# Optimization experiments

Measured on AMD Instinct MI355X. Metric: run time of the kernel, lower is better.

## Reference

```python
import jax, jax.numpy as jnp
import numpy as np

B, L, I, H, O = 32, 4096, 128, 256, 128
DELAY = 4  # delay-line length is DELAY+1


def setup_inputs() -> dict:
    key = jax.random.key(0)
    ks = jax.random.split(key, 9)
    s = 0.02
    return {
        "x": jax.random.normal(ks[0], (B, L, I), jnp.float32),
        # MGRUCell params (minimal-GRU: forget gate uses delayed state)
        "Wz": jax.random.normal(ks[1], (I, H), jnp.float32) * s,
        "Uz": jax.random.normal(ks[2], (H, H), jnp.float32) * s,
        "bz": jnp.zeros((H,), jnp.float32),
        "Wh": jax.random.normal(ks[3], (I, H), jnp.float32) * s,
        "Uh": jax.random.normal(ks[4], (H, H), jnp.float32) * s,
        "bh": jnp.zeros((H,), jnp.float32),
        # head: Linear(H, O)
        "Wo": jax.random.normal(ks[5], (H, O), jnp.float32) * s,
        "bo": jnp.zeros((O,), jnp.float32),
    }


def reference(x, Wz, Uz, bz, Wh, Uh, bh, Wo, bo):
    Bv, Lv, _ = x.shape
    Hv = Wz.shape[1]
    # precompute all input projections in two big GEMMs (time-parallel part)
    xz = jnp.einsum("bli,ih->blh", x, Wz) + bz  # [B,L,H]
    xh = jnp.einsum("bli,ih->blh", x, Wh) + bh  # [B,L,H]
    h0 = jnp.zeros((Bv, Hv), x.dtype)
    hist0 = jnp.zeros((DELAY + 1, Bv, Hv), x.dtype)  # delay line, hist[0] is oldest

    def step(carry, xs):
        h, hist = carry
        xz_t, xh_t = xs
        h_delay = hist[0]
        z = jax.nn.sigmoid(xz_t + h_delay @ Uz)          # gate from delayed state
        h_tilde = jnp.tanh(xh_t + (z * h) @ Uh)           # candidate (minimal-GRU)
        h_new = (1.0 - z) * h + z * h_tilde
        hist_new = jnp.concatenate([hist[1:], h_new[None]], axis=0)
        return (h_new, hist_new), h_new

    (_, _), hs = jax.lax.scan(
        step, (h0, hist0), (jnp.swapaxes(xz, 0, 1), jnp.swapaxes(xh, 0, 1))
    )  # hs: [L,B,H]
    # per-step Linear head, applied as one GEMM over all steps
    y = jnp.einsum("lbh,ho->blo", hs, Wo) + bo  # [B,L,O]
    return y
```

## Files before the change

kernel.cpp:

```cpp
#include <hip/hip_runtime.h>
#include <hip/hip_bf16.h>

typedef _Float16 half2v __attribute__((ext_vector_type(2)));
typedef _Float16 half8v __attribute__((ext_vector_type(8)));
typedef float float4v __attribute__((ext_vector_type(4)));
typedef unsigned int u32;
typedef unsigned short u16;

#define DEV static __device__ __forceinline__

DEV u32 pack2(float a, float b) {
  half2v h = { (_Float16)a, (_Float16)b };
  return __builtin_bit_cast(u32, h);
}
DEV half2v uph(u32 u) { return __builtin_bit_cast(half2v, u); }
DEV u16 ftoh16(float f) { return __builtin_bit_cast(u16, (_Float16)f); }
DEV float h16tof(u16 s) { return (float)__builtin_bit_cast(_Float16, s); }

#if __has_builtin(__builtin_amdgcn_fdot2)
DEV float fdot2(half2v a, half2v b, float c) { return __builtin_amdgcn_fdot2(a, b, c, false); }
#else
DEV float fdot2(half2v a, half2v b, float c) {
  return c + (float)a.x * (float)b.x + (float)a.y * (float)b.y;
}
#endif

DEV float fast_rcp(float x) { return __builtin_amdgcn_rcpf(x); }
DEV float sigmoid_f(float x) { return fast_rcp(1.f + exp2f(-1.4426950408889634f * x)); }
DEV float tanh_f(float x) {
  float e = exp2f(x * 2.8853900817779268f);
  return 1.f - 2.f * fast_rcp(e + 1.f);
}

DEV void barrier_lgkm() {
  __asm__ __volatile__("s_waitcnt lgkmcnt(0)\ns_barrier" ::: "memory");
}

__global__ void prep_transpose(const float* __restrict__ Wz, const float* __restrict__ Wh,
                               const float* __restrict__ Wo, _Float16* __restrict__ Wzt,
                               _Float16* __restrict__ Wht, _Float16* __restrict__ Wot)
{
  const float* src; _Float16* dst; int R, C;
  if (blockIdx.y == 0)      { src = Wz; dst = Wzt; R = 128; C = 256; }
  else if (blockIdx.y == 1) { src = Wh; dst = Wht; R = 128; C = 256; }
  else                      { src = Wo; dst = Wot; R = 256; C = 128; }
  int total = R * C;
  for (int idx = blockIdx.x * blockDim.x + threadIdx.x; idx < total;
       idx += gridDim.x * blockDim.x) {
    int rr = idx / C, cc = idx % C;
    dst[(size_t)cc * R + rr] = (_Float16)src[idx];
  }
}

template <int K, int N, bool A_F32, bool OUT_F16>
__global__ __launch_bounds__(256, 2) void gemm_mfma(
    const void* __restrict__ A_, const _Float16* __restrict__ Bt,
    const float* __restrict__ bias, void* __restrict__ out)
{
  __shared__ _Float16 Blds[N * K];

  const int tid = threadIdx.x;
  constexpr int CHUNKS = K / 8;
  constexpr int ITER = (N * K / 8) / 256;
#pragma unroll
  for (int i = 0; i < ITER; ++i) {
    int idx = tid + i * 256;
    int n = idx / CHUNKS;
    int c = idx % CHUNKS;
    int cs = c ^ (n & 7);
    *(uint4*)(Blds + (size_t)n * K + cs * 8) =
        *(const uint4*)(Bt + (size_t)n * K + c * 8);
  }
  __syncthreads();

  const int w = tid >> 6, l = tid & 63;
  const int lm = l & 15, lq = l >> 4;
  const size_t m0 = (size_t)blockIdx.x * 128;

  float4v acc[2][N / 16] = {};

#pragma unroll
  for (int kk = 0; kk < K / 32; ++kk) {
    const int kbase = kk * 32 + lq * 8;
    half8v af[2];
#pragma unroll
    for (int ms = 0; ms < 2; ++ms) {
      const size_t row = m0 + (size_t)(w * 2 + ms) * 16 + lm;
      if constexpr (A_F32) {
        const float* ap = (const float*)A_ + row * K + kbase;
        float4 x0 = *(const float4*)ap;
        float4 x1 = *(const float4*)(ap + 4);
        af[ms] = half8v{(_Float16)x0.x, (_Float16)x0.y, (_Float16)x0.z, (_Float16)x0.w,
                        (_Float16)x1.x, (_Float16)x1.y, (_Float16)x1.z, (_Float16)x1.w};
      } else {
        af[ms] = *(const half8v*)((const _Float16*)A_ + row * K + kbase);
      }
    }
    const int c = kk * 4 + lq;
#pragma unroll
    for (int nt = 0; nt < N / 16; ++nt) {
      const int n = nt * 16 + lm;
      half8v bf = *(const half8v*)(Blds + (size_t)n * K + (c ^ (lm & 7)) * 8);
      acc[0][nt] = __builtin_amdgcn_mfma_f32_16x16x32_f16(af[0], bf, acc[0][nt], 0, 0, 0);
      acc[1][nt] = __builtin_amdgcn_mfma_f32_16x16x32_f16(af[1], bf, acc[1][nt], 0, 0, 0);
    }
  }

#pragma unroll
  for (int ms = 0; ms < 2; ++ms) {
    const size_t rowbase = m0 + (size_t)(w * 2 + ms) * 16 + lq * 4;
#pragma unroll
    for (int nt = 0; nt < N / 16; ++nt) {
      const int col = nt * 16 + lm;
      const float bcol = bias[col];
#pragma unroll
      for (int rr = 0; rr < 4; ++rr) {
        const size_t row = rowbase + rr;
        float v = acc[ms][nt][rr] + bcol;
        if constexpr (OUT_F16) ((_Float16*)out)[row * N + col] = (_Float16)v;
        else                   ((float*)out)[row * N + col] = v;
      }
    }
  }
}

__global__ __launch_bounds__(512, 2) void scan_kernel(
    const u32* __restrict__ xz32, const u32* __restrict__ xh32,
    const float* __restrict__ Uz, const float* __restrict__ Uh,
    u32* __restrict__ hsOut)
{
  const int b   = blockIdx.x;
  const int tid = threadIdx.x;
  const int w   = tid >> 6;
  const int l   = tid & 63;
  const int g   = w >> 2;
  const int wv  = w & 3;

  __shared__ __align__(16) u16 histS[8][264];
  __shared__ __align__(16) u16 zringS[8][264];
  __shared__ __align__(16) u16 zhS[8][264];
  __shared__ __align__(16) u16 xhS[2][1024];
  __shared__ __align__(16) u16 xzS[2][1024];

  uint4 W[32];

  const size_t xb32 = (size_t)b * 4096 * 128;
  const u16* xz16v = (const u16*)xz32;
  const int c   = wv * 64 + l;
  const int rr  = c >> 6;
  const int c4  = (c & 63) * 4;
  const int lm  = l & 15;
  const int q   = l >> 4;
  const int koff = q * 8;

  if (g == 0) {
#pragma unroll
    for (int nt = 0; nt < 4; ++nt) {
      const int cn = wv * 64 + nt * 16 + lm;
#pragma unroll
      for (int i = 0; i < 8; ++i) {
        u32 q2[4];
#pragma unroll
        for (int p2 = 0; p2 < 4; ++p2) {
          int k0 = q * 64 + i * 8 + 2 * p2;
          q2[p2] = pack2(Uh[(size_t)k0 * 256 + cn], Uh[(size_t)(k0 + 1) * 256 + cn]);
        }
        W[nt * 8 + i] = make_uint4(q2[0], q2[1], q2[2], q2[3]);
      }
    }
  } else {
#pragma unroll
    for (int kt = 0; kt < 8; ++kt)
#pragma unroll
      for (int nt = 0; nt < 4; ++nt) {
        u32 q2[4];
#pragma unroll
        for (int p2 = 0; p2 < 4; ++p2) {
          int k0 = kt * 32 + koff + 2 * p2;
          int cn = wv * 64 + nt * 16 + lm;
          q2[p2] = pack2(Uz[(size_t)k0 * 256 + cn], Uz[(size_t)(k0 + 1) * 256 + cn]);
        }
        W[kt * 4 + nt] = make_uint4(q2[0], q2[1], q2[2], q2[3]);
      }
  }

  for (int i = tid; i < 4 * 264; i += 512) (&histS[4][0])[i] = 0;
  for (int i = tid; i < 264; i += 512) zhS[0][i] = 0;

  if (g == 1) {
    uint2 xzv = *(const uint2*)&xz16v[((size_t)b * 4096 + rr) * 256 + c4];
    half2v a0 = uph(xzv.x), a1 = uph(xzv.y);
    u32 z01 = pack2(sigmoid_f((float)a0.x), sigmoid_f((float)a0.y));
    u32 z23 = pack2(sigmoid_f((float)a1.x), sigmoid_f((float)a1.y));
    *(uint2*)&zringS[rr][c4] = make_uint2(z01, z23);
    *(uint2*)&xhS[0][rr * 256 + c4] =
        *(const uint2*)&xh32[xb32 + (size_t)rr * 128 + (c & 63) * 2];
    *(uint2*)&xzS[0][rr * 256 + c4] =
        *(const uint2*)&xz16v[((size_t)b * 4096 + 4 + rr) * 256 + c4];
  }
  float h = 0.f;
  __syncthreads();

  for (int tb = 0; tb < 4096; tb += 4) {
    const int p = (tb >> 2) & 1;
    uint2 xhv, xzv2;
#pragma unroll
    for (int u = 0; u < 4; ++u) {
      const int t = tb + u;
      if (g == 0) {
        float xh_t = h16tof(xhS[p][u * 256 + c]);
        float z_t  = h16tof(zringS[t & 7][c]);
        const uint4* a4 = (const uint4*)&zhS[t & 7][q * 64];
        float s0 = 0.f, s1 = 0.f, s2 = 0.f, s3 = 0.f;
#pragma unroll
        for (int i = 0; i < 8; ++i) {
          uint4 A = a4[i];
          uint4 w0 = W[0 * 8 + i], w1 = W[1 * 8 + i];
          uint4 w2 = W[2 * 8 + i], w3 = W[3 * 8 + i];
          s0 = fdot2(uph(A.x), uph(w0.x), s0);
          s0 = fdot2(uph(A.y), uph(w0.y), s0);
          s0 = fdot2(uph(A.z), uph(w0.z), s0);
          s0 = fdot2(uph(A.w), uph(w0.w), s0);
          s1 = fdot2(uph(A.x), uph(w1.x), s1);
          s1 = fdot2(uph(A.y), uph(w1.y), s1);
          s1 = fdot2(uph(A.z), uph(w1.z), s1);
          s1 = fdot2(uph(A.w), uph(w1.w), s1);
          s2 = fdot2(uph(A.x), uph(w2.x), s2);
          s2 = fdot2(uph(A.y), uph(w2.y), s2);
          s2 = fdot2(uph(A.z), uph(w2.z), s2);
          s2 = fdot2(uph(A.w), uph(w2.w), s2);
          s3 = fdot2(uph(A.x), uph(w3.x), s3);
          s3 = fdot2(uph(A.y), uph(w3.y), s3);
          s3 = fdot2(uph(A.z), uph(w3.z), s3);
          s3 = fdot2(uph(A.w), uph(w3.w), s3);
        }
        float t0 = s0 + __shfl_xor(s0, 32);
        float t1 = s1 + __shfl_xor(s1, 32);
        float t2 = s2 + __shfl_xor(s2, 32);
        float t3 = s3 + __shfl_xor(s3, 32);
        float A2 = (q & 2) ? t2 : t0;
        float B2 = (q & 2) ? t3 : t1;
        A2 += __shfl_xor(A2, 16);
        B2 += __shfl_xor(B2, 16);
        float pre = (q & 1) ? B2 : A2;

        float htl = tanh_f(pre + xh_t);
        h += z_t * (htl - h);
        histS[t & 7][c] = ftoh16(h);
        if (u < 3) {
          float zn = h16tof(zringS[(t + 1) & 7][c]);
          zhS[(t + 1) & 7][c] = ftoh16(zn * h);
        }
        barrier_lgkm();
        if (u == 3) {
          float zn = h16tof(zringS[(t + 1) & 7][c]);
          zhS[(t + 1) & 7][c] = ftoh16(zn * h);
          barrier_lgkm();
        }
      } else {
        if (u == 0) {
          int rh = tb + 4 + rr; if (rh > 4095) rh = 4095;
          xhv = *(const uint2*)&xh32[xb32 + (size_t)rh * 128 + (c & 63) * 2];
          int rz = tb + 8 + rr; if (rz > 4095) rz = 4095;
          xzv2 = *(const uint2*)&xz16v[((size_t)b * 4096 + rz) * 256 + c4];
          if (tb > 0) {
            int ro = tb - 4 + rr;
            uint2 hv = *(const uint2*)&histS[ro & 7][c4];
            *(uint2*)&hsOut[xb32 + (size_t)ro * 128 + (c & 63) * 2] = hv;
          }
          barrier_lgkm();
        } else if (u == 2) {
          *(uint2*)&xhS[p ^ 1][rr * 256 + c4] = xhv;
          *(uint2*)&xzS[p ^ 1][rr * 256 + c4] = xzv2;
          barrier_lgkm();
        } else if (u == 3) {
          const int srow = (tb + 7 + (l & 3)) & 7;
          float4v acc4[4] = {};
#pragma unroll
          for (int kt = 0; kt < 8; ++kt) {
            half8v a = __builtin_bit_cast(
                half8v, *(const uint4*)&histS[srow][kt * 32 + koff]);
#pragma unroll
            for (int nt = 0; nt < 4; ++nt)
              acc4[nt] = __builtin_amdgcn_mfma_f32_16x16x32_f16(
                  a, __builtin_bit_cast(half8v, W[kt * 4 + nt]), acc4[nt], 0, 0, 0);
          }
          {
#pragma unroll
            for (int nt = 0; nt < 4; ++nt) {
              float4v a = acc4[nt];
              float pre = q == 0 ? a[0] : q == 1 ? a[1] : q == 2 ? a[2] : a[3];
              int cn = wv * 64 + nt * 16 + lm;
              float zv = sigmoid_f(pre + h16tof(xzS[p][q * 256 + cn]));
              zringS[(tb + 4 + q) & 7][cn] = ftoh16(zv);
            }
          }
          barrier_lgkm();
          barrier_lgkm();
        } else {
          barrier_lgkm();
        }
      }
    }
  }

  if (g == 1) {
    int ro = 4092 + rr;
    uint2 hv = *(const uint2*)&histS[ro & 7][c4];
    *(uint2*)&hsOut[xb32 + (size_t)ro * 128 + (c & 63) * 2] = hv;
  }
}

extern "C" void kernel_launch(void* const* d_in, const int* in_sizes, int n_in,
                              void* d_out, int out_size, void* d_ws, size_t ws_size,
                              hipStream_t stream)
{
  (void)in_sizes; (void)n_in; (void)out_size; (void)ws_size;
  const float* x  = (const float*)d_in[0];
  const float* Wz = (const float*)d_in[1];
  const float* Uz = (const float*)d_in[2];
  const float* bz = (const float*)d_in[3];
  const float* Wh = (const float*)d_in[4];
  const float* Uh = (const float*)d_in[5];
  const float* bh = (const float*)d_in[6];
  const float* Wo = (const float*)d_in[7];
  const float* bo = (const float*)d_in[8];

  char* ws = (char*)d_ws;
  _Float16* Wzt  = (_Float16*)(ws);
  _Float16* Wht  = (_Float16*)(ws + (64 << 10));
  _Float16* Wot  = (_Float16*)(ws + (128 << 10));
  _Float16* xz16 = (_Float16*)(ws + (256 << 10));
  _Float16* xh16 = (_Float16*)(ws + (256 << 10) + (size_t)64 * 1024 * 1024);

  _Float16* hs16 = (_Float16*)d_out;

  prep_transpose<<<dim3(32, 3), 256, 0, stream>>>(Wz, Wh, Wo, Wzt, Wht, Wot);
  gemm_mfma<128, 256, true, true><<<1024, 256, 0, stream>>>(x, Wzt, bz, xz16);
  gemm_mfma<128, 256, true, true><<<1024, 256, 0, stream>>>(x, Wht, bh, xh16);
  scan_kernel<<<32, 512, 0, stream>>>((const u32*)xz16, (const u32*)xh16,
                                      Uz, Uh, (u32*)d_out);
  gemm_mfma<256, 128, false, false><<<1024, 256, 0, stream>>>(hs16, Wot, bo, d_out);
}
```

Before: 2.900 ms.

## Process two batch rows per scan block to interleave independent recurrences

```diff
diff --git a/kernel.cpp b/kernel.cpp
--- a/kernel.cpp
+++ b/kernel.cpp
@@ -124,27 +124,28 @@
   }
 }
 
-__global__ __launch_bounds__(512, 2) void scan_kernel(
+__global__ __launch_bounds__(512, 1) void scan_kernel(
     const u32* __restrict__ xz32, const u32* __restrict__ xh32,
     const float* __restrict__ Uz, const float* __restrict__ Uh,
     u32* __restrict__ hsOut)
 {
-  const int b   = blockIdx.x;
   const int tid = threadIdx.x;
   const int w   = tid >> 6;
   const int l   = tid & 63;
   const int g   = w >> 2;
   const int wv  = w & 3;
 
-  __shared__ __align__(16) u16 histS[8][264];
-  __shared__ __align__(16) u16 zringS[8][264];
-  __shared__ __align__(16) u16 zhS[8][264];
-  __shared__ __align__(16) u16 xhS[2][1024];
-  __shared__ __align__(16) u16 xzS[2][1024];
+  __shared__ __align__(16) u16 histS[2][8][264];
+  __shared__ __align__(16) u16 zringS[2][8][264];
+  __shared__ __align__(16) u16 zhS[2][8][264];
+  __shared__ __align__(16) u16 xhS[2][2][1024];
+  __shared__ __align__(16) u16 xzS[2][2][1024];
 
   uint4 W[32];
 
-  const size_t xb32 = (size_t)b * 4096 * 128;
+  const int b0 = blockIdx.x * 2, b1 = b0 + 1;
+  const size_t xbA = (size_t)b0 * 4096 * 128;
+  const size_t xbB = (size_t)b1 * 4096 * 128;
   const u16* xz16v = (const u16*)xz32;
   const int c   = wv * 64 + l;
   const int rr  = c >> 6;
@@ -184,115 +185,170 @@
       }
   }
 
-  for (int i = tid; i < 4 * 264; i += 512) (&histS[4][0])[i] = 0;
-  for (int i = tid; i < 264; i += 512) zhS[0][i] = 0;
+#pragma unroll
+  for (int s = 0; s < 2; ++s) {
+    for (int i = tid; i < 4 * 264; i += 512) (&histS[s][4][0])[i] = 0;
+    for (int i = tid; i < 264; i += 512) zhS[s][0][i] = 0;
+  }
 
   if (g == 1) {
-    uint2 xzv = *(const uint2*)&xz16v[((size_t)b * 4096 + rr) * 256 + c4];
-    half2v a0 = uph(xzv.x), a1 = uph(xzv.y);
-    u32 z01 = pack2(sigmoid_f((float)a0.x), sigmoid_f((float)a0.y));
-    u32 z23 = pack2(sigmoid_f((float)a1.x), sigmoid_f((float)a1.y));
-    *(uint2*)&zringS[rr][c4] = make_uint2(z01, z23);
-    *(uint2*)&xhS[0][rr * 256 + c4] =
-        *(const uint2*)&xh32[xb32 + (size_t)rr * 128 + (c & 63) * 2];
-    *(uint2*)&xzS[0][rr * 256 + c4] =
-        *(const uint2*)&xz16v[((size_t)b * 4096 + 4 + rr) * 256 + c4];
-  }
-  float h = 0.f;
+#pragma unroll
+    for (int s = 0; s < 2; ++s) {
+      const size_t xb = s ? xbB : xbA;
+      const size_t bt = (size_t)(s ? b1 : b0) * 4096;
+      uint2 xzv = *(const uint2*)&xz16v[(bt + rr) * 256 + c4];
+      half2v a0 = uph(xzv.x), a1 = uph(xzv.y);
+      u32 z01 = pack2(sigmoid_f((float)a0.x), sigmoid_f((float)a0.y));
+      u32 z23 = pack2(sigmoid_f((float)a1.x), sigmoid_f((float)a1.y));
+      *(uint2*)&zringS[s][rr][c4] = make_uint2(z01, z23);
+      *(uint2*)&xhS[s][0][rr * 256 + c4] =
+          *(const uint2*)&xh32[xb + (size_t)rr * 128 + (c & 63) * 2];
+      *(uint2*)&xzS[s][0][rr * 256 + c4] =
+          *(const uint2*)&xz16v[(bt + 4 + rr) * 256 + c4];
+    }
+  }
+  float hA = 0.f, hB = 0.f;
   __syncthreads();
 
   for (int tb = 0; tb < 4096; tb += 4) {
     const int p = (tb >> 2) & 1;
-    uint2 xhv, xzv2;
+    uint2 xhvA, xzvA, xhvB, xzvB;
 #pragma unroll
     for (int u = 0; u < 4; ++u) {
       const int t = tb + u;
       if (g == 0) {
-        float xh_t = h16tof(xhS[p][u * 256 + c]);
-        float z_t  = h16tof(zringS[t & 7][c]);
-        const uint4* a4 = (const uint4*)&zhS[t & 7][q * 64];
-        float s0 = 0.f, s1 = 0.f, s2 = 0.f, s3 = 0.f;
+        float xh_tA = h16tof(xhS[0][p][u * 256 + c]);
+        float xh_tB = h16tof(xhS[1][p][u * 256 + c]);
+        float z_tA  = h16tof(zringS[0][t & 7][c]);
+        float z_tB  = h16tof(zringS[1][t & 7][c]);
+        u16 znA = 0, znB = 0;
+        if (u < 3) {
+          znA = zringS[0][(t + 1) & 7][c];
+          znB = zringS[1][(t + 1) & 7][c];
+        }
+        const uint4* a4A = (const uint4*)&zhS[0][t & 7][q * 64];
+        const uint4* a4B = (const uint4*)&zhS[1][t & 7][q * 64];
+        float sA0 = 0.f, sA1 = 0.f, sA2 = 0.f, sA3 = 0.f;
+        float sB0 = 0.f, sB1 = 0.f, sB2 = 0.f, sB3 = 0.f;
 #pragma unroll
         for (int i = 0; i < 8; ++i) {
-          uint4 A = a4[i];
+          uint4 A = a4A[i];
+          uint4 Bv = a4B[i];
           uint4 w0 = W[0 * 8 + i], w1 = W[1 * 8 + i];
           uint4 w2 = W[2 * 8 + i], w3 = W[3 * 8 + i];
-          s0 = fdot2(uph(A.x), uph(w0.x), s0);
-          s0 = fdot2(uph(A.y), uph(w0.y), s0);
-          s0 = fdot2(uph(A.z), uph(w0.z), s0);
-          s0 = fdot2(uph(A.w), uph(w0.w), s0);
-          s1 = fdot2(uph(A.x), uph(w1.x), s1);
-          s1 = fdot2(uph(A.y), uph(w1.y), s1);
-          s1 = fdot2(uph(A.z), uph(w1.z), s1);
-          s1 = fdot2(uph(A.w), uph(w1.w), s1);
-          s2 = fdot2(uph(A.x), uph(w2.x), s2);
-          s2 = fdot2(uph(A.y), uph(w2.y), s2);
-          s2 = fdot2(uph(A.z), uph(w2.z), s2);
-          s2 = fdot2(uph(A.w), uph(w2.w), s2);
-          s3 = fdot2(uph(A.x), uph(w3.x), s3);
-          s3 = fdot2(uph(A.y), uph(w3.y), s3);
-          s3 = fdot2(uph(A.z), uph(w3.z), s3);
-          s3 = fdot2(uph(A.w), uph(w3.w), s3);
-        }
-        float t0 = s0 + __shfl_xor(s0, 32);
-        float t1 = s1 + __shfl_xor(s1, 32);
-        float t2 = s2 + __shfl_xor(s2, 32);
-        float t3 = s3 + __shfl_xor(s3, 32);
-        float A2 = (q & 2) ? t2 : t0;
-        float B2 = (q & 2) ? t3 : t1;
-        A2 += __shfl_xor(A2, 16);
-        B2 += __shfl_xor(B2, 16);
-        float pre = (q & 1) ? B2 : A2;
-
-        float htl = tanh_f(pre + xh_t);
-        h += z_t * (htl - h);
-        histS[t & 7][c] = ftoh16(h);
+          sA0 = fdot2(uph(A.x), uph(w0.x), sA0);
+          sA0 = fdot2(uph(A.y), uph(w0.y), sA0);
+          sA0 = fdot2(uph(A.z), uph(w0.z), sA0);
+          sA0 = fdot2(uph(A.w), uph(w0.w), sA0);
+          sB0 = fdot2(uph(Bv.x), uph(w0.x), sB0);
+          sB0 = fdot2(uph(Bv.y), uph(w0.y), sB0);
+          sB0 = fdot2(uph(Bv.z), uph(w0.z), sB0);
+          sB0 = fdot2(uph(Bv.w), uph(w0.w), sB0);
+          sA1 = fdot2(uph(A.x), uph(w1.x), sA1);
+          sA1 = fdot2(uph(A.y), uph(w1.y), sA1);
+          sA1 = fdot2(uph(A.z), uph(w1.z), sA1);
+          sA1 = fdot2(uph(A.w), uph(w1.w), sA1);
+          sB1 = fdot2(uph(Bv.x), uph(w1.x), sB1);
+          sB1 = fdot2(uph(Bv.y), uph(w1.y), sB1);
+          sB1 = fdot2(uph(Bv.z), uph(w1.z), sB1);
+          sB1 = fdot2(uph(Bv.w), uph(w1.w), sB1);
+          sA2 = fdot2(uph(A.x), uph(w2.x), sA2);
+          sA2 = fdot2(uph(A.y), uph(w2.y), sA2);
+          sA2 = fdot2(uph(A.z), uph(w2.z), sA2);
+          sA2 = fdot2(uph(A.w), uph(w2.w), sA2);
+          sB2 = fdot2(uph(Bv.x), uph(w2.x), sB2);
+          sB2 = fdot2(uph(Bv.y), uph(w2.y), sB2);
+          sB2 = fdot2(uph(Bv.z), uph(w2.z), sB2);
+          sB2 = fdot2(uph(Bv.w), uph(w2.w), sB2);
+          sA3 = fdot2(uph(A.x), uph(w3.x), sA3);
+          sA3 = fdot2(uph(A.y), uph(w3.y), sA3);
+          sA3 = fdot2(uph(A.z), uph(w3.z), sA3);
+          sA3 = fdot2(uph(A.w), uph(w3.w), sA3);
+          sB3 = fdot2(uph(Bv.x), uph(w3.x), sB3);
+          sB3 = fdot2(uph(Bv.y), uph(w3.y), sB3);
+          sB3 = fdot2(uph(Bv.z), uph(w3.z), sB3);
+          sB3 = fdot2(uph(Bv.w), uph(w3.w), sB3);
+        }
+        float tA0 = sA0 + __shfl_xor(sA0, 32);
+        float tA1 = sA1 + __shfl_xor(sA1, 32);
+        float tA2 = sA2 + __shfl_xor(sA2, 32);
+        float tA3 = sA3 + __shfl_xor(sA3, 32);
+        float tB0 = sB0 + __shfl_xor(sB0, 32);
+        float tB1 = sB1 + __shfl_xor(sB1, 32);
+        float tB2 = sB2 + __shfl_xor(sB2, 32);
+        float tB3 = sB3 + __shfl_xor(sB3, 32);
+        float cA0 = (q & 2) ? tA2 : tA0;
+        float cA1 = (q & 2) ? tA3 : tA1;
+        float cB0 = (q & 2) ? tB2 : tB0;
+        float cB1 = (q & 2) ? tB3 : tB1;
+        cA0 += __shfl_xor(cA0, 16);
+        cA1 += __shfl_xor(cA1, 16);
+        cB0 += __shfl_xor(cB0, 16);
+        cB1 += __shfl_xor(cB1, 16);
+        float preA = (q & 1) ? cA1 : cA0;
+        float preB = (q & 1) ? cB1 : cB0;
+
+        float htlA = tanh_f(preA + xh_tA);
+        float htlB = tanh_f(preB + xh_tB);
+        hA += z_tA * (htlA - hA);
+        hB += z_tB * (htlB - hB);
+        histS[0][t & 7][c] = ftoh16(hA);
+        histS[1][t & 7][c] = ftoh16(hB);
         if (u < 3) {
-          float zn = h16tof(zringS[(t + 1) & 7][c]);
-          zhS[(t + 1) & 7][c] = ftoh16(zn * h);
+          zhS[0][(t + 1) & 7][c] = ftoh16(h16tof(znA) * hA);
+          zhS[1][(t + 1) & 7][c] = ftoh16(h16tof(znB) * hB);
         }
         barrier_lgkm();
         if (u == 3) {
-          float zn = h16tof(zringS[(t + 1) & 7][c]);
-          zhS[(t + 1) & 7][c] = ftoh16(zn * h);
+          float zn0 = h16tof(zringS[0][(t + 1) & 7][c]);
+          float zn1 = h16tof(zringS[1][(t + 1) & 7][c]);
+          zhS[0][(t + 1) & 7][c] = ftoh16(zn0 * hA);
+          zhS[1][(t + 1) & 7][c] = ftoh16(zn1 * hB);
           barrier_lgkm();
         }
       } else {
         if (u == 0) {
           int rh = tb + 4 + rr; if (rh > 4095) rh = 4095;
-          xhv = *(const uint2*)&xh32[xb32 + (size_t)rh * 128 + (c & 63) * 2];
           int rz = tb + 8 + rr; if (rz > 4095) rz = 4095;
-          xzv2 = *(const uint2*)&xz16v[((size_t)b * 4096 + rz) * 256 + c4];
+          xhvA = *(const uint2*)&xh32[xbA + (size_t)rh * 128 + (c & 63) * 2];
+          xhvB = *(const uint2*)&xh32[xbB + (size_t)rh * 128 + (c & 63) * 2];
+          xzvA = *(const uint2*)&xz16v[((size_t)b0 * 4096 + rz) * 256 + c4];
+          xzvB = *(const uint2*)&xz16v[((size_t)b1 * 4096 + rz) * 256 + c4];
           if (tb > 0) {
             int ro = tb - 4 + rr;
-            uint2 hv = *(const uint2*)&histS[ro & 7][c4];
-            *(uint2*)&hsOut[xb32 + (size_t)ro * 128 + (c & 63) * 2] = hv;
+            uint2 hvA = *(const uint2*)&histS[0][ro & 7][c4];
+            uint2 hvB = *(const uint2*)&histS[1][ro & 7][c4];
+            *(uint2*)&hsOut[xbA + (size_t)ro * 128 + (c & 63) * 2] = hvA;
+            *(uint2*)&hsOut[xbB + (size_t)ro * 128 + (c & 63) * 2] = hvB;
           }
           barrier_lgkm();
         } else if (u == 2) {
-          *(uint2*)&xhS[p ^ 1][rr * 256 + c4] = xhv;
-          *(uint2*)&xzS[p ^ 1][rr * 256 + c4] = xzv2;
+          *(uint2*)&xhS[0][p ^ 1][rr * 256 + c4] = xhvA;
+          *(uint2*)&xhS[1][p ^ 1][rr * 256 + c4] = xhvB;
+          *(uint2*)&xzS[0][p ^ 1][rr * 256 + c4] = xzvA;
+          *(uint2*)&xzS[1][p ^ 1][rr * 256 + c4] = xzvB;
           barrier_lgkm();
         } else if (u == 3) {
           const int srow = (tb + 7 + (l & 3)) & 7;
-          float4v acc4[4] = {};
-#pragma unroll
-          for (int kt = 0; kt < 8; ++kt) {
-            half8v a = __builtin_bit_cast(
-                half8v, *(const uint4*)&histS[srow][kt * 32 + koff]);
-#pragma unroll
-            for (int nt = 0; nt < 4; ++nt)
-              acc4[nt] = __builtin_amdgcn_mfma_f32_16x16x32_f16(
-                  a, __builtin_bit_cast(half8v, W[kt * 4 + nt]), acc4[nt], 0, 0, 0);
-          }
-          {
+#pragma unroll
+          for (int s = 0; s < 2; ++s) {
+            float4v acc4[4] = {};
+#pragma unroll
+            for (int kt = 0; kt < 8; ++kt) {
+              half8v a = __builtin_bit_cast(
+                  half8v, *(const uint4*)&histS[s][srow][kt * 32 + koff]);
+#pragma unroll
+              for (int nt = 0; nt < 4; ++nt)
+                acc4[nt] = __builtin_amdgcn_mfma_f32_16x16x32_f16(
+                    a, __builtin_bit_cast(half8v, W[kt * 4 + nt]), acc4[nt], 0, 0, 0);
+            }
 #pragma unroll
             for (int nt = 0; nt < 4; ++nt) {
               float4v a = acc4[nt];
               float pre = q == 0 ? a[0] : q == 1 ? a[1] : q == 2 ? a[2] : a[3];
               int cn = wv * 64 + nt * 16 + lm;
-              float zv = sigmoid_f(pre + h16tof(xzS[p][q * 256 + cn]));
-              zringS[(tb + 4 + q) & 7][cn] = ftoh16(zv);
+              float zv = sigmoid_f(pre + h16tof(xzS[s][p][q * 256 + cn]));
+              zringS[s][(tb + 4 + q) & 7][cn] = ftoh16(zv);
             }
           }
           barrier_lgkm();
@@ -306,8 +362,10 @@
 
   if (g == 1) {
     int ro = 4092 + rr;
-    uint2 hv = *(const uint2*)&histS[ro & 7][c4];
-    *(uint2*)&hsOut[xb32 + (size_t)ro * 128 + (c & 63) * 2] = hv;
+    uint2 hvA = *(const uint2*)&histS[0][ro & 7][c4];
+    uint2 hvB = *(const uint2*)&histS[1][ro & 7][c4];
+    *(uint2*)&hsOut[xbA + (size_t)ro * 128 + (c & 63) * 2] = hvA;
+    *(uint2*)&hsOut[xbB + (size_t)ro * 128 + (c & 63) * 2] = hvB;
   }
 }
 
@@ -338,7 +396,7 @@
   prep_transpose<<<dim3(32, 3), 256, 0, stream>>>(Wz, Wh, Wo, Wzt, Wht, Wot);
   gemm_mfma<128, 256, true, true><<<1024, 256, 0, stream>>>(x, Wzt, bz, xz16);
   gemm_mfma<128, 256, true, true><<<1024, 256, 0, stream>>>(x, Wht, bh, xh16);
-  scan_kernel<<<32, 512, 0, stream>>>((const u32*)xz16, (const u32*)xh16,
+  scan_kernel<<<16, 512, 0, stream>>>((const u32*)xz16, (const u32*)xh16,
                                       Uz, Uh, (u32*)d_out);
   gemm_mfma<256, 128, false, false><<<1024, 256, 0, stream>>>(hs16, Wot, bo, d_out);
 }
```

Result: slower. 4.880 ms (+68.3%).

## Merge specialized warp groups so all warps share recurrence and gate work

Applied to the files above, without the earlier changes.

```diff
diff --git a/kernel.cpp b/kernel.cpp
--- a/kernel.cpp
+++ b/kernel.cpp
@@ -124,7 +124,7 @@
   }
 }
 
-__global__ __launch_bounds__(512, 2) void scan_kernel(
+__global__ __launch_bounds__(512, 1) void scan_kernel(
     const u32* __restrict__ xz32, const u32* __restrict__ xh32,
     const float* __restrict__ Uz, const float* __restrict__ Uh,
     u32* __restrict__ hsOut)
@@ -133,181 +133,152 @@
   const int tid = threadIdx.x;
   const int w   = tid >> 6;
   const int l   = tid & 63;
-  const int g   = w >> 2;
-  const int wv  = w & 3;
+  const int lm  = l & 15;
+  const int q   = l >> 4;
 
   __shared__ __align__(16) u16 histS[8][264];
   __shared__ __align__(16) u16 zringS[8][264];
-  __shared__ __align__(16) u16 zhS[8][264];
+  __shared__ __align__(16) u16 zhS[8][4][72];
   __shared__ __align__(16) u16 xhS[2][1024];
   __shared__ __align__(16) u16 xzS[2][1024];
 
-  uint4 W[32];
+  uint4 WH0[8], WH1[8];
+  uint4 WZ[16];
 
   const size_t xb32 = (size_t)b * 4096 * 128;
-  const u16* xz16v = (const u16*)xz32;
-  const int c   = wv * 64 + l;
-  const int rr  = c >> 6;
-  const int c4  = (c & 63) * 4;
-  const int lm  = l & 15;
-  const int q   = l >> 4;
-  const int koff = q * 8;
-
-  if (g == 0) {
-#pragma unroll
-    for (int nt = 0; nt < 4; ++nt) {
-      const int cn = wv * 64 + nt * 16 + lm;
-#pragma unroll
-      for (int i = 0; i < 8; ++i) {
-        u32 q2[4];
-#pragma unroll
-        for (int p2 = 0; p2 < 4; ++p2) {
-          int k0 = q * 64 + i * 8 + 2 * p2;
-          q2[p2] = pack2(Uh[(size_t)k0 * 256 + cn], Uh[(size_t)(k0 + 1) * 256 + cn]);
-        }
-        W[nt * 8 + i] = make_uint4(q2[0], q2[1], q2[2], q2[3]);
-      }
-    }
-  } else {
-#pragma unroll
-    for (int kt = 0; kt < 8; ++kt)
-#pragma unroll
-      for (int nt = 0; nt < 4; ++nt) {
-        u32 q2[4];
-#pragma unroll
-        for (int p2 = 0; p2 < 4; ++p2) {
-          int k0 = kt * 32 + koff + 2 * p2;
-          int cn = wv * 64 + nt * 16 + lm;
-          q2[p2] = pack2(Uz[(size_t)k0 * 256 + cn], Uz[(size_t)(k0 + 1) * 256 + cn]);
-        }
-        W[kt * 4 + nt] = make_uint4(q2[0], q2[1], q2[2], q2[3]);
-      }
-  }
+  const size_t bt4  = (size_t)b * 4096;
+  const int c   = w * 32 + (l & 31);
+  const int csl = c >> 6;
+  const int co  = c & 63;
+  const int cw0 = w * 32 + lm;
+  const int cw1 = cw0 + 16;
+  const int srr = tid >> 7;
+  const int scc = tid & 127;
+
+#pragma unroll
+  for (int i = 0; i < 8; ++i) {
+    u32 qa[4], qb[4];
+#pragma unroll
+    for (int p2 = 0; p2 < 4; ++p2) {
+      int k0 = q * 64 + i * 8 + 2 * p2;
+      qa[p2] = pack2(Uh[(size_t)k0 * 256 + cw0], Uh[(size_t)(k0 + 1) * 256 + cw0]);
+      qb[p2] = pack2(Uh[(size_t)k0 * 256 + cw1], Uh[(size_t)(k0 + 1) * 256 + cw1]);
+    }
+    WH0[i] = make_uint4(qa[0], qa[1], qa[2], qa[3]);
+    WH1[i] = make_uint4(qb[0], qb[1], qb[2], qb[3]);
+  }
+#pragma unroll
+  for (int kt = 0; kt < 8; ++kt)
+#pragma unroll
+    for (int nt = 0; nt < 2; ++nt) {
+      u32 q2[4];
+#pragma unroll
+      for (int p2 = 0; p2 < 4; ++p2) {
+        int k0 = kt * 32 + q * 8 + 2 * p2;
+        int cn = w * 32 + nt * 16 + lm;
+        q2[p2] = pack2(Uz[(size_t)k0 * 256 + cn], Uz[(size_t)(k0 + 1) * 256 + cn]);
+      }
+      WZ[kt * 2 + nt] = make_uint4(q2[0], q2[1], q2[2], q2[3]);
+    }
 
   for (int i = tid; i < 4 * 264; i += 512) (&histS[4][0])[i] = 0;
-  for (int i = tid; i < 264; i += 512) zhS[0][i] = 0;
-
-  if (g == 1) {
-    uint2 xzv = *(const uint2*)&xz16v[((size_t)b * 4096 + rr) * 256 + c4];
-    half2v a0 = uph(xzv.x), a1 = uph(xzv.y);
-    u32 z01 = pack2(sigmoid_f((float)a0.x), sigmoid_f((float)a0.y));
-    u32 z23 = pack2(sigmoid_f((float)a1.x), sigmoid_f((float)a1.y));
-    *(uint2*)&zringS[rr][c4] = make_uint2(z01, z23);
-    *(uint2*)&xhS[0][rr * 256 + c4] =
-        *(const uint2*)&xh32[xb32 + (size_t)rr * 128 + (c & 63) * 2];
-    *(uint2*)&xzS[0][rr * 256 + c4] =
-        *(const uint2*)&xz16v[((size_t)b * 4096 + 4 + rr) * 256 + c4];
+  for (int i = tid; i < 4 * 72; i += 512) (&zhS[0][0][0])[i] = 0;
+
+  {
+    u32 xzv = xz32[(bt4 + srr) * 128 + scc];
+    half2v a0 = uph(xzv);
+    *(u32*)&zringS[srr][scc * 2] = pack2(sigmoid_f((float)a0.x), sigmoid_f((float)a0.y));
+    *(u32*)&xhS[0][srr * 256 + scc * 2] = xh32[xb32 + (size_t)srr * 128 + scc];
+    *(u32*)&xzS[0][srr * 256 + scc * 2] = xz32[(bt4 + 4 + srr) * 128 + scc];
   }
   float h = 0.f;
   __syncthreads();
 
   for (int tb = 0; tb < 4096; tb += 4) {
     const int p = (tb >> 2) & 1;
-    uint2 xhv, xzv2;
+    u32 xhv, xzv;
 #pragma unroll
     for (int u = 0; u < 4; ++u) {
       const int t = tb + u;
-      if (g == 0) {
-        float xh_t = h16tof(xhS[p][u * 256 + c]);
-        float z_t  = h16tof(zringS[t & 7][c]);
-        const uint4* a4 = (const uint4*)&zhS[t & 7][q * 64];
-        float s0 = 0.f, s1 = 0.f, s2 = 0.f, s3 = 0.f;
-#pragma unroll
-        for (int i = 0; i < 8; ++i) {
-          uint4 A = a4[i];
-          uint4 w0 = W[0 * 8 + i], w1 = W[1 * 8 + i];
-          uint4 w2 = W[2 * 8 + i], w3 = W[3 * 8 + i];
-          s0 = fdot2(uph(A.x), uph(w0.x), s0);
-          s0 = fdot2(uph(A.y), uph(w0.y), s0);
-          s0 = fdot2(uph(A.z), uph(w0.z), s0);
-          s0 = fdot2(uph(A.w), uph(w0.w), s0);
-          s1 = fdot2(uph(A.x), uph(w1.x), s1);
-          s1 = fdot2(uph(A.y), uph(w1.y), s1);
-          s1 = fdot2(uph(A.z), uph(w1.z), s1);
-          s1 = fdot2(uph(A.w), uph(w1.w), s1);
-          s2 = fdot2(uph(A.x), uph(w2.x), s2);
-          s2 = fdot2(uph(A.y), uph(w2.y), s2);
-          s2 = fdot2(uph(A.z), uph(w2.z), s2);
-          s2 = fdot2(uph(A.w), uph(w2.w), s2);
-          s3 = fdot2(uph(A.x), uph(w3.x), s3);
-          s3 = fdot2(uph(A.y), uph(w3.y), s3);
-          s3 = fdot2(uph(A.z), uph(w3.z), s3);
-          s3 = fdot2(uph(A.w), uph(w3.w), s3);
+
+      if (u == 0) {
+        int rh = tb + 4 + srr; if (rh > 4095) rh = 4095;
+        int rz = tb + 8 + srr; if (rz > 4095) rz = 4095;
+        xhv = xh32[xb32 + (size_t)rh * 128 + scc];
+        xzv = xz32[(bt4 + rz) * 128 + scc];
+        if (tb > 0) {
+          int ro = tb - 4 + srr;
+          hsOut[xb32 + (size_t)ro * 128 + scc] = *(const u32*)&histS[ro & 7][scc * 2];
         }
-        float t0 = s0 + __shfl_xor(s0, 32);
-        float t1 = s1 + __shfl_xor(s1, 32);
-        float t2 = s2 + __shfl_xor(s2, 32);
-        float t3 = s3 + __shfl_xor(s3, 32);
-        float A2 = (q & 2) ? t2 : t0;
-        float B2 = (q & 2) ? t3 : t1;
-        A2 += __shfl_xor(A2, 16);
-        B2 += __shfl_xor(B2, 16);
-        float pre = (q & 1) ? B2 : A2;
-
-        float htl = tanh_f(pre + xh_t);
-        h += z_t * (htl - h);
-        histS[t & 7][c] = ftoh16(h);
-        if (u < 3) {
-          float zn = h16tof(zringS[(t + 1) & 7][c]);
-          zhS[(t + 1) & 7][c] = ftoh16(zn * h);
+      } else if (u == 2) {
+        *(u32*)&xhS[p ^ 1][srr * 256 + scc * 2] = xhv;
+        *(u32*)&xzS[p ^ 1][srr * 256 + scc * 2] = xzv;
+      }
+
+      float4v acc0 = {}, acc1 = {};
+      if (u == 3) {
+        const int srow = (tb + 7 + (l & 3)) & 7;
+        const int koff = q * 8;
+#pragma unroll
+        for (int kt = 0; kt < 8; ++kt) {
+          half8v a = __builtin_bit_cast(
+              half8v, *(const uint4*)&histS[srow][kt * 32 + koff]);
+          acc0 = __builtin_amdgcn_mfma_f32_16x16x32_f16(
+              a, __builtin_bit_cast(half8v, WZ[kt * 2 + 0]), acc0, 0, 0, 0);
+          acc1 = __builtin_amdgcn_mfma_f32_16x16x32_f16(
+              a, __builtin_bit_cast(half8v, WZ[kt * 2 + 1]), acc1, 0, 0, 0);
         }
+      }
+
+      float xh_t = h16tof(xhS[p][u * 256 + c]);
+      float z_t  = h16tof(zringS[t & 7][c]);
+      u16 zn = (u < 3) ? zringS[(t + 1) & 7][c] : (u16)0;
+      const uint4* a4 = (const uint4*)&zhS[t & 7][q][0];
+      float s0 = 0.f, s1 = 0.f;
+#pragma unroll
+      for (int i = 0; i < 8; ++i) {
+        uint4 A = a4[i];
+        uint4 w0 = WH0[i], w1 = WH1[i];
+        s0 = fdot2(uph(A.x), uph(w0.x), s0);
+        s0 = fdot2(uph(A.y), uph(w0.y), s0);
+        s0 = fdot2(uph(A.z), uph(w0.z), s0);
+        s0 = fdot2(uph(A.w), uph(w0.w), s0);
+        s1 = fdot2(uph(A.x), uph(w1.x), s1);
+        s1 = fdot2(uph(A.y), uph(w1.y), s1);
+        s1 = fdot2(uph(A.z), uph(w1.z), s1);
+        s1 = fdot2(uph(A.w), uph(w1.w), s1);
+      }
+      s0 += __shfl_xor(s0, 32);
+      s1 += __shfl_xor(s1, 32);
+      s0 += __shfl_xor(s0, 16);
+      s1 += __shfl_xor(s1, 16);
+      float pre = (q & 1) ? s1 : s0;
+      float htl = tanh_f(pre + xh_t);
+      h += z_t * (htl - h);
+      histS[t & 7][c] = ftoh16(h);
+
+      if (u < 3) {
+        zhS[(t + 1) & 7][csl][co] = ftoh16(h16tof(zn) * h);
         barrier_lgkm();
-        if (u == 3) {
-          float zn = h16tof(zringS[(t + 1) & 7][c]);
-          zhS[(t + 1) & 7][c] = ftoh16(zn * h);
-          barrier_lgkm();
-        }
       } else {
-        if (u == 0) {
-          int rh = tb + 4 + rr; if (rh > 4095) rh = 4095;
-          xhv = *(const uint2*)&xh32[xb32 + (size_t)rh * 128 + (c & 63) * 2];
-          int rz = tb + 8 + rr; if (rz > 4095) rz = 4095;
-          xzv2 = *(const uint2*)&xz16v[((size_t)b * 4096 + rz) * 256 + c4];
-          if (tb > 0) {
-            int ro = tb - 4 + rr;
-            uint2 hv = *(const uint2*)&histS[ro & 7][c4];
-            *(uint2*)&hsOut[xb32 + (size_t)ro * 128 + (c & 63) * 2] = hv;
-          }
-          barrier_lgkm();
-        } else if (u == 2) {
-          *(uint2*)&xhS[p ^ 1][rr * 256 + c4] = xhv;
-          *(uint2*)&xzS[p ^ 1][rr * 256 + c4] = xzv2;
-          barrier_lgkm();
-        } else if (u == 3) {
-          const int srow = (tb + 7 + (l & 3)) & 7;
-          float4v acc4[4] = {};
-#pragma unroll
-          for (int kt = 0; kt < 8; ++kt) {
-            half8v a = __builtin_bit_cast(
-                half8v, *(const uint4*)&histS[srow][kt * 32 + koff]);
-#pragma unroll
-            for (int nt = 0; nt < 4; ++nt)
-              acc4[nt] = __builtin_amdgcn_mfma_f32_16x16x32_f16(
-                  a, __builtin_bit_cast(half8v, W[kt * 4 + nt]), acc4[nt], 0, 0, 0);
-          }
-          {
-#pragma unroll
-            for (int nt = 0; nt < 4; ++nt) {
-              float4v a = acc4[nt];
-              float pre = q == 0 ? a[0] : q == 1 ? a[1] : q == 2 ? a[2] : a[3];
-              int cn = wv * 64 + nt * 16 + lm;
-              float zv = sigmoid_f(pre + h16tof(xzS[p][q * 256 + cn]));
-              zringS[(tb + 4 + q) & 7][cn] = ftoh16(zv);
-            }
-          }
-          barrier_lgkm();
-          barrier_lgkm();
-        } else {
-          barrier_lgkm();
-        }
-      }
-    }
-  }
-
-  if (g == 1) {
-    int ro = 4092 + rr;
-    uint2 hv = *(const uint2*)&histS[ro & 7][c4];
-    *(uint2*)&hsOut[xb32 + (size_t)ro * 128 + (c & 63) * 2] = hv;
+        float e0 = q == 0 ? acc0[0] : q == 1 ? acc0[1] : q == 2 ? acc0[2] : acc0[3];
+        float e1 = q == 0 ? acc1[0] : q == 1 ? acc1[1] : q == 2 ? acc1[2] : acc1[3];
+        int cn0 = w * 32 + lm, cn1 = cn0 + 16;
+        float z0 = sigmoid_f(e0 + h16tof(xzS[p][q * 256 + cn0]));
+        float z1 = sigmoid_f(e1 + h16tof(xzS[p][q * 256 + cn1]));
+        zringS[(tb + 4 + q) & 7][cn0] = ftoh16(z0);
+        zringS[(tb + 4 + q) & 7][cn1] = ftoh16(z1);
+        barrier_lgkm();
+        float znb = h16tof(zringS[(tb + 4) & 7][c]);
+        zhS[(tb + 4) & 7][csl][co] = ftoh16(znb * h);
+        barrier_lgkm();
+      }
+    }
+  }
+
+  {
+    int ro = 4092 + srr;
+    hsOut[xb32 + (size_t)ro * 128 + scc] = *(const u32*)&histS[ro & 7][scc * 2];
   }
 }
 
```

Result: no change. 2.944 ms (+1.5%).
